# Kernel optimization log

Measured on AMD Instinct MI355X. Metric: run time of the kernel, lower is better.

The kernel has to match this reference:

```python
import jax, jax.numpy as jnp
import numpy as np

B, H, S, D = 2, 16, 2048, 64

def setup_inputs() -> dict:
    key = jax.random.key(0)
    kq, kk, kv = jax.random.split(key, 3)
    q = jax.random.normal(kq, (B, H, S, D), dtype=jnp.float32)
    k = jax.random.normal(kk, (B, H, S, D), dtype=jnp.float32)
    v = jax.random.normal(kv, (B, H, S, D), dtype=jnp.float32)
    # causal mask, True = attend
    mask = jnp.broadcast_to(jnp.tril(jnp.ones((S, S), dtype=bool)), (B, H, S, S))
    return {"q": q, "k": k, "v": v, "mask": mask}

def reference(q, k, v, mask):
    dim = q.shape[-1]
    scale = 1.0 / jnp.sqrt(jnp.asarray(dim, q.dtype))
    scores = jnp.einsum('bhqd,bhkd->bhqk', q, k) * scale  # [B,H,S,S]
    scores = jnp.where(mask, scores, jnp.finfo(scores.dtype).min)
    probs = jax.nn.softmax(scores, axis=-1)
    return jnp.einsum('bhqk,bhkd->bhqd', probs, v)
```

## Files before the change

kernel.cpp:

```cpp
#include <hip/hip_runtime.h>

#define B_   2
#define H_   16
#define S_   2048
#define D_   64
#define BQ   128
#define NW   8
#define QSCALE 0.18033688011112042f
#define DEFER_THR 8.0f

typedef _Float16 f16x8 __attribute__((ext_vector_type(8)));
typedef float    f32x4 __attribute__((ext_vector_type(4)));

typedef const unsigned int __attribute__((address_space(1))) gu32;
typedef unsigned int       __attribute__((address_space(3))) lu32;

#define KBYTES_PER_HEAD (S_ * 128)
#define WS_V_OFF ((size_t)B_ * H_ * KBYTES_PER_HEAD)
#define WS_NEED  (2 * WS_V_OFF)

__global__ __launch_bounds__(256) void prep_kv(const float* __restrict__ K,
                                               const float* __restrict__ V,
                                               char* __restrict__ ws)
{
    if (blockIdx.x < (B_ * H_ * S_ * 8) / 256) {
        const int gidx = blockIdx.x * 256 + threadIdx.x;
        const int gcol = gidx & 7;
        const int srow = gidx >> 3;
        const float4* src = (const float4*)(K + (size_t)srow * D_ + gcol * 8);
        float4 a = src[0], b = src[1];
        f16x8 h;
        h[0] = (_Float16)a.x; h[1] = (_Float16)a.y; h[2] = (_Float16)a.z; h[3] = (_Float16)a.w;
        h[4] = (_Float16)b.x; h[5] = (_Float16)b.y; h[6] = (_Float16)b.z; h[7] = (_Float16)b.w;
        const int s  = srow & (S_ - 1);
        const int bh = srow >> 11;
        size_t off = (size_t)bh * KBYTES_PER_HEAD + (size_t)(s >> 6) * 8192
                   + (s & 63) * 128 + ((gcol ^ (s & 7)) << 4);
        *(f16x8*)(ws + off) = h;
    } else {
        __shared__ _Float16 Vl[64][72];
        const int tile = blockIdx.x - (B_ * H_ * S_ * 8) / 256;
        const int bh = tile >> 5, t = tile & 31;
        const float* vb = V + ((size_t)bh * S_ + t * 64) * D_;
        const int tid = threadIdx.x;
        #pragma unroll
        for (int it = 0; it < 2; ++it) {
            const int row = (tid >> 3) + it * 32;
            const int c8  = (tid & 7) * 8;
            const float4* p = (const float4*)(vb + row * D_ + c8);
            float4 a = p[0], b = p[1];
            f16x8 h;
            h[0] = (_Float16)a.x; h[1] = (_Float16)a.y; h[2] = (_Float16)a.z; h[3] = (_Float16)a.w;
            h[4] = (_Float16)b.x; h[5] = (_Float16)b.y; h[6] = (_Float16)b.z; h[7] = (_Float16)b.w;
            *(f16x8*)&Vl[row][c8] = h;
        }
        __syncthreads();
        char* out = ws + WS_V_OFF + (size_t)bh * KBYTES_PER_HEAD + t * 8192;
        #pragma unroll
        for (int it = 0; it < 2; ++it) {
            const int task = tid + it * 256;
            const int d = task >> 3, kg = task & 7;
            f16x8 h;
            #pragma unroll
            for (int j = 0; j < 8; ++j) h[j] = Vl[kg * 8 + j][d];
            *(f16x8*)(out + d * 128 + ((kg ^ (d & 7)) << 4)) = h;
        }
    }
}

template<bool MASK>
__device__ __forceinline__ void qk_tile(
    const _Float16* __restrict__ Kb, const f16x8 aq[2], f32x4 (&accS)[4],
    int g, int l15, int dq)
{
    const int rbase = 8 * (l15 >> 2) + (l15 & 3);
    #pragma unroll
    for (int s = 0; s < 4; ++s) accS[s] = (f32x4){0.f, 0.f, 0.f, 0.f};
    __builtin_amdgcn_s_setprio(1);
    #pragma unroll
    for (int sub = 0; sub < 4; ++sub) {
        if (MASK && (32 * (sub >> 1) + 4 * (sub & 1) > dq + 15)) continue;
        const int kr  = rbase + 4 * (sub & 1) + 32 * (sub >> 1);
        const int sxk = (l15 & 3) + 4 * (sub & 1);
        #pragma unroll
        for (int kc = 0; kc < 2; ++kc) {
            f16x8 ak = *(const f16x8*)(Kb + (kr * 64 + (((kc * 4 + g) ^ sxk) << 3)));
            accS[sub] = __builtin_amdgcn_mfma_f32_16x16x32_f16(ak, aq[kc], accS[sub], 0, 0, 0);
        }
    }
    __builtin_amdgcn_s_setprio(0);
}

template<bool MASK>
__device__ __forceinline__ void smpv_tile(
    const _Float16* __restrict__ SMb,
    f32x4 (&accS)[4], f32x4 accO[4], float& m_r, float& l_r,
    int g, int l15, int sx, int dq)
{
    const _Float16* Vb = SMb + 4096;

    auto msk = [&](int sub, int r) -> float {
        float s = accS[sub][r];
        if (MASK) {
            const int kk = 32 * (sub >> 1) + 8 * g + 4 * (sub & 1) + r;
            if (kk > dq + l15) s = -1e30f;
        }
        return s;
    };

    float pmax = -1e30f;
    #pragma unroll
    for (int sub = 0; sub < 4; ++sub)
        #pragma unroll
        for (int r = 0; r < 4; ++r) pmax = fmaxf(pmax, msk(sub, r));

    if (!__all(pmax <= m_r + DEFER_THR)) {
        float mx = pmax;
        mx = fmaxf(mx, __shfl_xor(mx, 16));
        mx = fmaxf(mx, __shfl_xor(mx, 32));
        const float mnew  = fmaxf(m_r, mx);
        const float alpha = __builtin_amdgcn_exp2f(m_r - mnew);
        l_r *= alpha;
        #pragma unroll
        for (int d = 0; d < 4; ++d)
            #pragma unroll
            for (int r = 0; r < 4; ++r) accO[d][r] *= alpha;
        m_r = mnew;
    }

    float rs = 0.f;
    f16x8 pb0, pb1;
    #pragma unroll
    for (int sub = 0; sub < 4; ++sub) {
        float p0 = __builtin_amdgcn_exp2f(msk(sub, 0) - m_r);
        float p1 = __builtin_amdgcn_exp2f(msk(sub, 1) - m_r);
        float p2 = __builtin_amdgcn_exp2f(msk(sub, 2) - m_r);
        float p3 = __builtin_amdgcn_exp2f(msk(sub, 3) - m_r);
        rs += (p0 + p1) + (p2 + p3);
        if (sub == 0) {
            pb0[0] = (_Float16)p0; pb0[1] = (_Float16)p1;
            pb0[2] = (_Float16)p2; pb0[3] = (_Float16)p3;
        } else if (sub == 1) {
            pb0[4] = (_Float16)p0; pb0[5] = (_Float16)p1;
            pb0[6] = (_Float16)p2; pb0[7] = (_Float16)p3;
        } else if (sub == 2) {
            pb1[0] = (_Float16)p0; pb1[1] = (_Float16)p1;
            pb1[2] = (_Float16)p2; pb1[3] = (_Float16)p3;
        } else {
            pb1[4] = (_Float16)p0; pb1[5] = (_Float16)p1;
            pb1[6] = (_Float16)p2; pb1[7] = (_Float16)p3;
        }
    }
    l_r += rs;

    __builtin_amdgcn_s_setprio(1);
    #pragma unroll
    for (int d = 0; d < 4; ++d) {
        f16x8 av0 = *(const f16x8*)(Vb + ((d * 16 + l15) * 64 + (((0 * 4 + g) ^ sx) << 3)));
        accO[d] = __builtin_amdgcn_mfma_f32_16x16x32_f16(av0, pb0, accO[d], 0, 0, 0);
        f16x8 av1 = *(const f16x8*)(Vb + ((d * 16 + l15) * 64 + (((1 * 4 + g) ^ sx) << 3)));
        accO[d] = __builtin_amdgcn_mfma_f32_16x16x32_f16(av1, pb1, accO[d], 0, 0, 0);
    }
    __builtin_amdgcn_s_setprio(0);
}

__global__ __launch_bounds__(512, 4) void attn_main(
    const float* __restrict__ Q, const char* __restrict__ ws, float* __restrict__ O)
{
    __shared__ _Float16 SM[3][8192];

    const int tid  = threadIdx.x;
    const int lane = tid & 63;
    const int w    = tid >> 6;
    const int g    = lane >> 4;
    const int l15  = lane & 15;
    const int sx   = l15 & 7;

    const int id    = blockIdx.x;
    const int bh    = id & 31;
    const int qi    = id >> 5;
    const int qt    = (id < 256) ? (15 - qi) : (qi - 8);
    const int qbase = qt * BQ;

    const char* kbase = ws + (size_t)bh * KBYTES_PER_HEAD;
    const char* vbase = ws + WS_V_OFF + (size_t)bh * KBYTES_PER_HEAD;

    f16x8 aq[2];
    {
        const float* qrow = Q + ((size_t)bh * S_ + qbase + w * 16 + l15) * D_;
        #pragma unroll
        for (int kc = 0; kc < 2; ++kc) {
            const float4* p = (const float4*)(qrow + kc * 32 + g * 8);
            float4 x0 = p[0], x1 = p[1];
            f16x8 h;
            h[0] = (_Float16)(x0.x * QSCALE); h[1] = (_Float16)(x0.y * QSCALE);
            h[2] = (_Float16)(x0.z * QSCALE); h[3] = (_Float16)(x0.w * QSCALE);
            h[4] = (_Float16)(x1.x * QSCALE); h[5] = (_Float16)(x1.y * QSCALE);
            h[6] = (_Float16)(x1.z * QSCALE); h[7] = (_Float16)(x1.w * QSCALE);
            aq[kc] = h;
        }
    }

    f32x4 accO[4];
    #pragma unroll
    for (int i = 0; i < 4; ++i) accO[i] = (f32x4){0.f, 0.f, 0.f, 0.f};
    float m_r = -1e30f, l_r = 0.f;
    f32x4 accSA[4], accSB[4];

    const int nt  = 2 * qt + 2;
    const int dqw = qbase + w * 16;

    _Float16* bQK = &SM[0][0];
    _Float16* bST = &SM[1][0];
    _Float16* bPV = &SM[2][0];

    auto STAGE = [&](int t, _Float16* dst) {
        #pragma unroll
        for (int i = 0; i < 2; ++i) {
            const int c = w * 2 + i;
            const char* src = (c < 8 ? kbase + (size_t)t * 8192 + c * 1024
                                     : vbase + (size_t)t * 8192 + (c - 8) * 1024) + lane * 16;
            __builtin_amdgcn_global_load_lds((gu32*)src, (lu32*)(dst + c * 512), 16, 0, 0);
        }
    };
    auto SYNC = []() {
        asm volatile("s_waitcnt vmcnt(0)" ::: "memory");
        __builtin_amdgcn_s_barrier();
    };
    auto ROT = [&]() { _Float16* tmp = bPV; bPV = bQK; bQK = bST; bST = tmp; };

    STAGE(0, bQK);

    SYNC();
    STAGE(1, bST);
    if (qt == 0) qk_tile<true >(bQK, aq, accSA, g, l15, dqw);
    else         qk_tile<false>(bQK, aq, accSA, g, l15, 0);
    ROT();

    SYNC();
    if (nt > 2) STAGE(2, bST);
    if (qt == 0) {
        qk_tile<true >(bQK, aq, accSB, g, l15, dqw - 64);
        smpv_tile<true >(bPV, accSA, accO, m_r, l_r, g, l15, sx, dqw);
    } else {
        qk_tile<false>(bQK, aq, accSB, g, l15, 0);
        smpv_tile<false>(bPV, accSA, accO, m_r, l_r, g, l15, sx, 0);
    }
    ROT();

    for (int i = 1; i < qt; ++i) {
        const int t0 = 2 * i;
        SYNC();
        STAGE(t0 + 1, bST);
        qk_tile<false>(bQK, aq, accSA, g, l15, 0);
        smpv_tile<false>(bPV, accSB, accO, m_r, l_r, g, l15, sx, 0);
        ROT();
        SYNC();
        STAGE(t0 + 2, bST);
        qk_tile<false>(bQK, aq, accSB, g, l15, 0);
        smpv_tile<false>(bPV, accSA, accO, m_r, l_r, g, l15, sx, 0);
        ROT();
    }

    if (qt >= 1) {
        SYNC();
        STAGE(nt - 1, bST);
        qk_tile<true >(bQK, aq, accSA, g, l15, dqw - (nt - 2) * 64);
        smpv_tile<false>(bPV, accSB, accO, m_r, l_r, g, l15, sx, 0);
        ROT();
        SYNC();
        qk_tile<true >(bQK, aq, accSB, g, l15, dqw - (nt - 1) * 64);
        smpv_tile<true >(bPV, accSA, accO, m_r, l_r, g, l15, sx, dqw - (nt - 2) * 64);
        ROT();
    }

    smpv_tile<true>(bPV, accSB, accO, m_r, l_r, g, l15, sx, dqw - (nt - 1) * 64);

    float l = l_r;
    l += __shfl_xor(l, 16);
    l += __shfl_xor(l, 32);
    const float inv = 1.0f / l;
    float* orow = O + ((size_t)bh * S_ + qbase + w * 16 + l15) * D_;
    #pragma unroll
    for (int d = 0; d < 4; ++d) {
        f32x4 o = accO[d] * inv;
        *(f32x4*)&orow[d * 16 + g * 4] = o;
    }
}

extern "C" void kernel_launch(void* const* d_in, const int* in_sizes, int n_in,
                              void* d_out, int out_size, void* d_ws, size_t ws_size,
                              hipStream_t stream) {
    const float* q = (const float*)d_in[0];
    const float* k = (const float*)d_in[1];
    const float* v = (const float*)d_in[2];
    float* o = (float*)d_out;
    char* ws = (char*)d_ws;

    if (ws_size < WS_NEED) return;

    const int kblocks = (B_ * H_ * S_ * 8) / 256;
    const int vblocks = B_ * H_ * (S_ / 64);
    prep_kv<<<kblocks + vblocks, 256, 0, stream>>>(k, v, ws);
    attn_main<<<(S_ / BQ) * B_ * H_, 512, 0, stream>>>(q, ws, o);
}
```

Baseline: 48.01 us.

## Split K/V staging into separate ring buffers and process two tiles per barrier

```diff
diff --git a/kernel.cpp b/kernel.cpp
--- a/kernel.cpp
+++ b/kernel.cpp
@@ -93,12 +93,10 @@
 
 template<bool MASK>
 __device__ __forceinline__ void smpv_tile(
-    const _Float16* __restrict__ SMb,
+    const _Float16* __restrict__ Vb,
     f32x4 (&accS)[4], f32x4 accO[4], float& m_r, float& l_r,
     int g, int l15, int sx, int dq)
 {
-    const _Float16* Vb = SMb + 4096;
-
     auto msk = [&](int sub, int r) -> float {
         float s = accS[sub][r];
         if (MASK) {
@@ -167,7 +165,8 @@
 __global__ __launch_bounds__(512, 4) void attn_main(
     const float* __restrict__ Q, const char* __restrict__ ws, float* __restrict__ O)
 {
-    __shared__ _Float16 SM[3][8192];
+    __shared__ _Float16 KBuf[4][4096];
+    __shared__ _Float16 VBuf[5][4096];
 
     const int tid  = threadIdx.x;
     const int lane = tid & 63;
@@ -209,72 +208,53 @@
 
     const int nt  = 2 * qt + 2;
     const int dqw = qbase + w * 16;
-
-    _Float16* bQK = &SM[0][0];
-    _Float16* bST = &SM[1][0];
-    _Float16* bPV = &SM[2][0];
-
-    auto STAGE = [&](int t, _Float16* dst) {
-        #pragma unroll
-        for (int i = 0; i < 2; ++i) {
-            const int c = w * 2 + i;
-            const char* src = (c < 8 ? kbase + (size_t)t * 8192 + c * 1024
-                                     : vbase + (size_t)t * 8192 + (c - 8) * 1024) + lane * 16;
-            __builtin_amdgcn_global_load_lds((gu32*)src, (lu32*)(dst + c * 512), 16, 0, 0);
-        }
+    const int dqA = dqw - (nt - 2) * 64;
+    const int dqB = dqw - (nt - 1) * 64;
+
+    _Float16 *kb0 = &KBuf[0][0], *kb1 = &KBuf[1][0], *kb2 = &KBuf[2][0], *kb3 = &KBuf[3][0];
+    _Float16 *vb0 = &VBuf[0][0], *vb1 = &VBuf[1][0], *vb2 = &VBuf[2][0],
+             *vb3 = &VBuf[3][0], *vb4 = &VBuf[4][0];
+
+    auto STAGE_K = [&](int t, _Float16* dst) {
+        const char* src = kbase + (size_t)t * 8192 + w * 1024 + lane * 16;
+        __builtin_amdgcn_global_load_lds((gu32*)src, (lu32*)(dst + w * 512), 16, 0, 0);
+    };
+    auto STAGE_V = [&](int t, _Float16* dst) {
+        const char* src = vbase + (size_t)t * 8192 + w * 1024 + lane * 16;
+        __builtin_amdgcn_global_load_lds((gu32*)src, (lu32*)(dst + w * 512), 16, 0, 0);
     };
     auto SYNC = []() {
         asm volatile("s_waitcnt vmcnt(0)" ::: "memory");
         __builtin_amdgcn_s_barrier();
     };
-    auto ROT = [&]() { _Float16* tmp = bPV; bPV = bQK; bQK = bST; bST = tmp; };
-
-    STAGE(0, bQK);
+    auto ROT = [&]() {
+        _Float16* t0 = kb0; _Float16* t1 = kb1;
+        kb0 = kb2; kb1 = kb3; kb2 = t0; kb3 = t1;
+        _Float16* u0 = vb0; _Float16* u1 = vb1;
+        vb0 = vb2; vb1 = vb3; vb2 = vb4; vb3 = u0; vb4 = u1;
+    };
+
+    STAGE_K(0, kb0); STAGE_V(0, vb1);
+    STAGE_K(1, kb1); STAGE_V(1, vb2);
+
+    for (int i = 0; i < qt; ++i) {
+        SYNC();
+        STAGE_K(2 * i + 2, kb2); STAGE_V(2 * i + 2, vb3);
+        STAGE_K(2 * i + 3, kb3); STAGE_V(2 * i + 3, vb4);
+        qk_tile<false>(kb0, aq, accSA, g, l15, 0);
+        if (i > 0) smpv_tile<false>(vb0, accSB, accO, m_r, l_r, g, l15, sx, 0);
+        qk_tile<false>(kb1, aq, accSB, g, l15, 0);
+        smpv_tile<false>(vb1, accSA, accO, m_r, l_r, g, l15, sx, 0);
+        ROT();
+    }
 
     SYNC();
-    STAGE(1, bST);
-    if (qt == 0) qk_tile<true >(bQK, aq, accSA, g, l15, dqw);
-    else         qk_tile<false>(bQK, aq, accSA, g, l15, 0);
+    qk_tile<true>(kb0, aq, accSA, g, l15, dqA);
+    if (qt > 0) smpv_tile<false>(vb0, accSB, accO, m_r, l_r, g, l15, sx, 0);
+    qk_tile<true>(kb1, aq, accSB, g, l15, dqB);
+    smpv_tile<true>(vb1, accSA, accO, m_r, l_r, g, l15, sx, dqA);
     ROT();
-
-    SYNC();
-    if (nt > 2) STAGE(2, bST);
-    if (qt == 0) {
-        qk_tile<true >(bQK, aq, accSB, g, l15, dqw - 64);
-        smpv_tile<true >(bPV, accSA, accO, m_r, l_r, g, l15, sx, dqw);
-    } else {
-        qk_tile<false>(bQK, aq, accSB, g, l15, 0);
-        smpv_tile<false>(bPV, accSA, accO, m_r, l_r, g, l15, sx, 0);
-    }
-    ROT();
-
-    for (int i = 1; i < qt; ++i) {
-        const int t0 = 2 * i;
-        SYNC();
-        STAGE(t0 + 1, bST);
-        qk_tile<false>(bQK, aq, accSA, g, l15, 0);
-        smpv_tile<false>(bPV, accSB, accO, m_r, l_r, g, l15, sx, 0);
-        ROT();
-        SYNC();
-        STAGE(t0 + 2, bST);
-        qk_tile<false>(bQK, aq, accSB, g, l15, 0);
-        smpv_tile<false>(bPV, accSA, accO, m_r, l_r, g, l15, sx, 0);
-        ROT();
-    }
-
-    if (qt >= 1) {
-        SYNC();
-        STAGE(nt - 1, bST);
-        qk_tile<true >(bQK, aq, accSA, g, l15, dqw - (nt - 2) * 64);
-        smpv_tile<false>(bPV, accSB, accO, m_r, l_r, g, l15, sx, 0);
-        ROT();
-        SYNC();
-        qk_tile<true >(bQK, aq, accSB, g, l15, dqw - (nt - 1) * 64);
-        smpv_tile<true >(bPV, accSA, accO, m_r, l_r, g, l15, sx, dqw - (nt - 2) * 64);
-        ROT();
-    }
-
-    smpv_tile<true>(bPV, accSB, accO, m_r, l_r, g, l15, sx, dqw - (nt - 1) * 64);
+    smpv_tile<true>(vb0, accSB, accO, m_r, l_r, g, l15, sx, dqB);
 
     float l = l_r;
     l += __shfl_xor(l, 16);
```

Result: faster. 44.85 us (median of 2 runs) (-6.6%).
